# Performance work log

Measured on AMD Instinct MI355X. Metric: run time of the kernel, lower is better.

## Reference

```python
import jax, jax.numpy as jnp
from jax import lax
import numpy as np

GAMMA = 1e-4  # RBF bandwidth (init kwarg gamma)

def setup_inputs() -> dict:
    key = jax.random.key(0)
    ks = jax.random.split(key, 6)
    B, H, W = 2048, 64, 64
    P, D = 4096, 4096  # D = 4 * (H//2) * (W//2)
    NC = 10
    x = jax.random.normal(ks[0], (B, 1, H, W), dtype=jnp.float32)
    prototypes = jax.random.normal(ks[1], (P, D), dtype=jnp.float32) * 0.5
    conv_w = jax.random.normal(ks[2], (4, 1, 2, 2), dtype=jnp.float32) * 0.5
    conv_b = jax.random.normal(ks[3], (4,), dtype=jnp.float32) * 0.1
    head_w = jax.random.normal(ks[4], (NC, P), dtype=jnp.float32) * (1.0 / np.sqrt(P))
    head_b = jax.random.normal(ks[5], (NC,), dtype=jnp.float32) * 0.1
    return {"x": x, "prototypes": prototypes, "conv_w": conv_w,
            "conv_b": conv_b, "head_w": head_w, "head_b": head_b}

def reference(x, prototypes, conv_w, conv_b, head_w, head_b):
    # 2x2 stride-2 conv: [B,1,H,W] -> [B,4,H/2,W/2]
    feats = lax.conv_general_dilated(
        x, conv_w, window_strides=(2, 2), padding="VALID",
        dimension_numbers=("NCHW", "OIHW", "NCHW"))
    feats = feats + conv_b[None, :, None, None]
    B = feats.shape[0]
    feats = feats.reshape(B, -1)  # [B, D]
    # Pairwise squared distance via ||f||^2 + ||p||^2 - 2 f.p (no [B,P,D] blowup)
    f2 = jnp.sum(feats * feats, axis=1, keepdims=True)          # [B,1]
    p2 = jnp.sum(prototypes * prototypes, axis=1)[None, :]      # [1,P]
    d2 = jnp.maximum(f2 + p2 - 2.0 * feats @ prototypes.T, 0.0)  # [B,P]
    kernel_vals = jnp.exp(-GAMMA * d2)
    logits = kernel_vals @ head_w.T + head_b
    return jax.nn.log_softmax(logits, axis=-1)
```

## Files before the change

kernel.cpp:

```cpp
#include <hip/hip_runtime.h>
#include <hip/hip_bf16.h>
#include <stdint.h>

#define GAMMA 1e-4f

typedef int i32x4 __attribute__((ext_vector_type(4)));
typedef int i32x8 __attribute__((ext_vector_type(8)));
typedef float f32x4 __attribute__((ext_vector_type(4)));

__device__ __forceinline__ float bf2f(unsigned short u) {
  unsigned int x = ((unsigned int)u) << 16;
  float f; __builtin_memcpy(&f, &x, 4);
  return f;
}

__device__ __forceinline__ unsigned char f2e4m3(float x) {
  float a = fabsf(x);
  unsigned char s = x < 0.f ? 0x80 : 0;
  a = fminf(a, 448.f);
  if (a < 0.015625f) {
    int q = (int)rintf(a * 512.f);
    return s | (unsigned char)q;
  }
  unsigned int u; __builtin_memcpy(&u, &a, 4);
  u += 0x7FFFFu + ((u >> 20) & 1);
  u &= 0xFFF00000u;
  int e2 = (int)(u >> 23) - 127;
  unsigned int mant = (u >> 20) & 7;
  return s | (unsigned char)(((e2 + 7) << 3) | mant);
}

__device__ __forceinline__ unsigned int pack4(float a, float b, float c, float d) {
  return (unsigned)f2e4m3(a) | ((unsigned)f2e4m3(b) << 8) |
         ((unsigned)f2e4m3(c) << 16) | ((unsigned)f2e4m3(d) << 24);
}

__global__ __launch_bounds__(256) void prep_k(
    const float* __restrict__ x, const float* __restrict__ cw,
    const float* __restrict__ cb, unsigned char* __restrict__ fA8,
    float* __restrict__ f2, const float* __restrict__ pr,
    unsigned char* __restrict__ pB8, float* __restrict__ p2) {
  const int tid = threadIdx.x;
  __shared__ float red[4];
  if (blockIdx.x < 4096) {
    const int j = blockIdx.x;
    const float4* src = (const float4*)(pr + (size_t)j * 4096);
    float ssq = 0.f;
    unsigned int w4[4];
#pragma unroll
    for (int k = 0; k < 4; k++) {
      float4 v = src[tid * 4 + k];
      ssq += v.x * v.x + v.y * v.y + v.z * v.z + v.w * v.w;
      w4[k] = pack4(v.x, v.y, v.z, v.w);
    }
    *(uint4*)(pB8 + (size_t)j * 4096 + tid * 16) = make_uint4(w4[0], w4[1], w4[2], w4[3]);
    for (int off = 32; off > 0; off >>= 1) ssq += __shfl_down(ssq, off);
    if ((tid & 63) == 0) red[tid >> 6] = ssq;
    __syncthreads();
    if (tid == 0) p2[j] = red[0] + red[1] + red[2] + red[3];
  } else {
    const int b = blockIdx.x - 4096;
    __shared__ float swb[20];
    if (tid < 16) swb[tid] = cw[tid];
    else if (tid < 20) swb[tid] = cb[tid - 16];
    __syncthreads();
    float w[16], bias[4];
#pragma unroll
    for (int i = 0; i < 16; i++) w[i] = swb[i];
#pragma unroll
    for (int c = 0; c < 4; c++) bias[c] = swb[16 + c];
    const float* xb = x + (size_t)b * 4096;
    unsigned char* fb8 = fA8 + (size_t)b * 4096;
    const int p0 = tid * 4;
    const int h = p0 >> 5, w0 = p0 & 31;
    const float* r0 = xb + (2 * h) * 64 + 2 * w0;
    const float* r1 = r0 + 64;
    float4 a0 = *(const float4*)r0, a1 = *(const float4*)(r0 + 4);
    float4 c0 = *(const float4*)r1, c1 = *(const float4*)(r1 + 4);
    float ssq = 0.f;
#pragma unroll
    for (int c = 0; c < 4; c++) {
      float w00 = w[c * 4], w01 = w[c * 4 + 1], w10 = w[c * 4 + 2], w11 = w[c * 4 + 3];
      float v0 = bias[c] + a0.x * w00 + a0.y * w01 + c0.x * w10 + c0.y * w11;
      float v1 = bias[c] + a0.z * w00 + a0.w * w01 + c0.z * w10 + c0.w * w11;
      float v2 = bias[c] + a1.x * w00 + a1.y * w01 + c1.x * w10 + c1.y * w11;
      float v3 = bias[c] + a1.z * w00 + a1.w * w01 + c1.z * w10 + c1.w * w11;
      ssq += v0 * v0 + v1 * v1 + v2 * v2 + v3 * v3;
      *(unsigned int*)(fb8 + c * 1024 + p0) = pack4(v0, v1, v2, v3);
    }
    for (int off = 32; off > 0; off >>= 1) ssq += __shfl_down(ssq, off);
    if ((tid & 63) == 0) red[tid >> 6] = ssq;
    __syncthreads();
    if (tid == 0) f2[b] = red[0] + red[1] + red[2] + red[3];
  }
}

#define SWZA(o) ((o) ^ ((((o) >> 12) & 1) << 4))
#define SWZB(o) ((o) ^ ((((o) >> 13) & 1) << 4))
#define TILE_BYTES 49152

#define GLDS(gsrc, ldst)                                                    \
  __builtin_amdgcn_global_load_lds(                                         \
      (__attribute__((address_space(1))) void*)(void*)(gsrc),               \
      (__attribute__((address_space(3))) void*)(ldst), 16, 0, 0)

#define MFMA8(a, b, c)                                                      \
  __builtin_amdgcn_mfma_scale_f32_16x16x128_f8f6f4(                         \
      (a), (b), (c), 0, 0, 0, 0x7f7f7f7fu, 0, 0x7f7f7f7fu)

__device__ __forceinline__ i32x8 read32(const char* p0, const char* p1) {
  i32x4 lo = *(const i32x4*)p0;
  i32x4 hi = *(const i32x4*)p1;
  return __builtin_shufflevector(lo, hi, 0, 1, 2, 3, 4, 5, 6, 7);
}

#define TBODY(PTN, PTS, CA0, CA1, CA2, CA3, CB0, CB1, CB2, CB3,             \
              NA0, NA1, NA2, NA3, NB0, NB1, NB2, NB3, KB)                   \
  {                                                                         \
    asm volatile("s_waitcnt vmcnt(0)" ::: "memory");                        \
    __builtin_amdgcn_sched_barrier(0);                                      \
    __builtin_amdgcn_s_barrier();                                           \
    asm volatile("s_waitcnt lgkmcnt(0)" ::: "memory");                      \
    __builtin_amdgcn_sched_barrier(0);                                      \
    NA0 = read32((PTN) + arlo[0], (PTN) + arhi[0]);                         \
    NA1 = read32((PTN) + arlo[1], (PTN) + arhi[1]);                         \
    NA2 = read32((PTN) + arlo[2], (PTN) + arhi[2]);                         \
    NA3 = read32((PTN) + arlo[3], (PTN) + arhi[3]);                         \
    NB0 = read32((PTN) + brlo[0], (PTN) + brhi[0]);                         \
    NB1 = read32((PTN) + brlo[1], (PTN) + brhi[1]);                         \
    GLDS(agp[0] + (KB), (PTS) + aoff[0]);                                   \
    GLDS(agp[1] + (KB), (PTS) + aoff[1]);                                   \
    GLDS(bgp[0] + (KB), (PTS) + 16384 + boff[0]);                           \
    __builtin_amdgcn_sched_barrier(0);                                      \
    __builtin_amdgcn_s_setprio(1);                                          \
    acc[0][0] = MFMA8(CA0, CB0, acc[0][0]);                                 \
    acc[0][1] = MFMA8(CA0, CB1, acc[0][1]);                                 \
    acc[1][0] = MFMA8(CA1, CB0, acc[1][0]);                                 \
    acc[1][1] = MFMA8(CA1, CB1, acc[1][1]);                                 \
    acc[2][0] = MFMA8(CA2, CB0, acc[2][0]);                                 \
    acc[2][1] = MFMA8(CA2, CB1, acc[2][1]);                                 \
    acc[3][0] = MFMA8(CA3, CB0, acc[3][0]);                                 \
    acc[3][1] = MFMA8(CA3, CB1, acc[3][1]);                                 \
    __builtin_amdgcn_s_setprio(0);                                          \
    __builtin_amdgcn_sched_barrier(0);                                      \
    NB2 = read32((PTN) + brlo[2], (PTN) + brhi[2]);                         \
    NB3 = read32((PTN) + brlo[3], (PTN) + brhi[3]);                         \
    GLDS(bgp[1] + (KB), (PTS) + 16384 + boff[1]);                           \
    GLDS(bgp[2] + (KB), (PTS) + 16384 + boff[2]);                           \
    GLDS(bgp[3] + (KB), (PTS) + 16384 + boff[3]);                           \
    __builtin_amdgcn_sched_barrier(0);                                      \
    __builtin_amdgcn_s_setprio(1);                                          \
    acc[0][2] = MFMA8(CA0, CB2, acc[0][2]);                                 \
    acc[0][3] = MFMA8(CA0, CB3, acc[0][3]);                                 \
    acc[1][2] = MFMA8(CA1, CB2, acc[1][2]);                                 \
    acc[1][3] = MFMA8(CA1, CB3, acc[1][3]);                                 \
    acc[2][2] = MFMA8(CA2, CB2, acc[2][2]);                                 \
    acc[2][3] = MFMA8(CA2, CB3, acc[2][3]);                                 \
    acc[3][2] = MFMA8(CA3, CB3, acc[3][2]);                                 \
    acc[3][3] = MFMA8(CA3, CB3, acc[3][3]);                                 \
    __builtin_amdgcn_s_setprio(0);                                          \
    __builtin_amdgcn_sched_barrier(0);                                      \
  }

__global__ __launch_bounds__(512, 1) void gemm_kv_k(
    const unsigned char* __restrict__ A, const unsigned char* __restrict__ B,
    const float* __restrict__ f2, const float* __restrict__ p2,
    __hip_bfloat16* __restrict__ kv) {
  __shared__ __align__(16) char lds[3 * TILE_BYTES];
  const int tid = threadIdx.x;
  const int wave = tid >> 6, lane = tid & 63;
  const int q = lane >> 4, l16 = lane & 15;
  const int wr = wave >> 2, wc = wave & 3;

  const int wg = blockIdx.x;
  const int xcd = wg & 7, loc = wg >> 3;
  const int bm = (xcd & 1) * 8 + (loc & 7);
  const int bn = (xcd >> 1) * 4 + (loc >> 3);

  const unsigned char* agp[2];
  const unsigned char* bgp[4];
  int aoff[2], boff[4];
#pragma unroll
  for (int i = 0; i < 2; i++) {
    int phys = (tid + i * 512) * 16;
    aoff[i] = phys;
    int lg = SWZA(phys);
    int kq = lg >> 12, rw = (lg & 4095) >> 5, kl = lg & 31;
    agp[i] = A + (size_t)(bm * 128 + rw) * 4096 + kq * 32 + kl;
  }
#pragma unroll
  for (int i = 0; i < 4; i++) {
    int phys = (tid + i * 512) * 16;
    boff[i] = phys;
    int lg = SWZB(phys);
    int kq = lg >> 13, rw = (lg & 8191) >> 5, kl = lg & 31;
    bgp[i] = B + (size_t)(bn * 256 + rw) * 4096 + kq * 32 + kl;
  }

  int arlo[4], arhi[4], brlo[4], brhi[4];
#pragma unroll
  for (int m = 0; m < 4; m++) {
    int lg = q * 4096 + (wr * 64 + m * 16 + l16) * 32;
    arlo[m] = SWZA(lg);
    arhi[m] = SWZA(lg + 16);
  }
#pragma unroll
  for (int n = 0; n < 4; n++) {
    int lg = q * 8192 + (wc * 64 + n * 16 + l16) * 32;
    brlo[n] = 16384 + SWZB(lg);
    brhi[n] = 16384 + SWZB(lg + 16);
  }

  f32x4 acc[4][4] = {};
  i32x8 Xa0, Xa1, Xa2, Xa3, Xb0, Xb1, Xb2, Xb3;
  i32x8 Ya0, Ya1, Ya2, Ya3, Yb0, Yb1, Yb2, Yb3;

  char* b0 = lds;
  char* b1 = lds + TILE_BYTES;
  char* b2 = lds + 2 * TILE_BYTES;

#pragma unroll
  for (int i = 0; i < 2; i++) GLDS(agp[i], b0 + aoff[i]);
#pragma unroll
  for (int i = 0; i < 4; i++) GLDS(bgp[i], b0 + 16384 + boff[i]);
#pragma unroll
  for (int i = 0; i < 2; i++) GLDS(agp[i] + 128, b1 + aoff[i]);
#pragma unroll
  for (int i = 0; i < 4; i++) GLDS(bgp[i] + 128, b1 + 16384 + boff[i]);
  asm volatile("s_waitcnt vmcnt(6)" ::: "memory");
  __builtin_amdgcn_s_barrier();

  Xa0 = read32(b0 + arlo[0], b0 + arhi[0]);
  Xa1 = read32(b0 + arlo[1], b0 + arhi[1]);
  Xa2 = read32(b0 + arlo[2], b0 + arhi[2]);
  Xa3 = read32(b0 + arlo[3], b0 + arhi[3]);
  Xb0 = read32(b0 + brlo[0], b0 + brhi[0]);
  Xb1 = read32(b0 + brlo[1], b0 + brhi[1]);
  Xb2 = read32(b0 + brlo[2], b0 + brhi[2]);
  Xb3 = read32(b0 + brlo[3], b0 + brhi[3]);

#pragma unroll 1
  for (int t = 0; t < 32; t += 2) {
    const int kb2 = ((t + 2) & 31) * 128;
    const int kb3 = ((t + 3) & 31) * 128;
    TBODY(b1, b2, Xa0, Xa1, Xa2, Xa3, Xb0, Xb1, Xb2, Xb3,
          Ya0, Ya1, Ya2, Ya3, Yb0, Yb1, Yb2, Yb3, kb2);
    TBODY(b2, b0, Ya0, Ya1, Ya2, Ya3, Yb0, Yb1, Yb2, Yb3,
          Xa0, Xa1, Xa2, Xa3, Xb0, Xb1, Xb2, Xb3, kb3);
    char* nb0 = b2; char* nb1 = b0; char* nb2 = b1;
    b0 = nb0; b1 = nb1; b2 = nb2;
  }

  asm volatile("s_waitcnt vmcnt(0) lgkmcnt(0)" ::: "memory");

  float p2v[4];
#pragma unroll
  for (int n = 0; n < 4; n++) p2v[n] = p2[bn * 256 + wc * 64 + n * 16 + l16];
#pragma unroll
  for (int m = 0; m < 4; m++) {
#pragma unroll
    for (int j = 0; j < 4; j++) {
      int grow = bm * 128 + wr * 64 + m * 16 + q * 4 + j;
      float f2v = f2[grow];
      __hip_bfloat16* kvp = kv + (size_t)grow * 4096 + bn * 256 + wc * 64 + l16;
#pragma unroll
      for (int n = 0; n < 4; n++) {
        float d2 = fmaxf(f2v + p2v[n] - 2.0f * acc[m][n][j], 0.f);
        kvp[n * 16] = __float2bfloat16(__expf(-GAMMA * d2));
      }
    }
  }
}

__global__ __launch_bounds__(256) void head_ls_k(
    const __hip_bfloat16* __restrict__ kv, const float* __restrict__ hw,
    const float* __restrict__ hb, float* __restrict__ out) {
  const int bb = blockIdx.x * 8;
  const int tid = threadIdx.x;
  float part[8][10];
#pragma unroll
  for (int r = 0; r < 8; r++)
#pragma unroll
    for (int c = 0; c < 10; c++) part[r][c] = 0.f;
#pragma unroll
  for (int k = 0; k < 4; k++) {
    int idx = tid + k * 256;
    float4 w[10];
#pragma unroll
    for (int c = 0; c < 10; c++) w[c] = *(const float4*)(hw + c * 4096 + idx * 4);
#pragma unroll
    for (int r = 0; r < 8; r++) {
      ushort4 v = ((const ushort4*)(kv + (size_t)(bb + r) * 4096))[idx];
      float a0 = bf2f(v.x), a1 = bf2f(v.y), a2 = bf2f(v.z), a3 = bf2f(v.w);
#pragma unroll
      for (int c = 0; c < 10; c++)
        part[r][c] += a0 * w[c].x + a1 * w[c].y + a2 * w[c].z + a3 * w[c].w;
    }
  }
#pragma unroll
  for (int r = 0; r < 8; r++)
#pragma unroll
    for (int c = 0; c < 10; c++)
      for (int off = 32; off > 0; off >>= 1) part[r][c] += __shfl_down(part[r][c], off);
  __shared__ float red[4][8][10];
  if ((tid & 63) == 0) {
#pragma unroll
    for (int r = 0; r < 8; r++)
#pragma unroll
      for (int c = 0; c < 10; c++) red[tid >> 6][r][c] = part[r][c];
  }
  __syncthreads();
  if (tid < 8) {
    const int r = tid;
    float l[10], m = -1e30f;
#pragma unroll
    for (int c = 0; c < 10; c++) {
      l[c] = red[0][r][c] + red[1][r][c] + red[2][r][c] + red[3][r][c] + hb[c];
      m = fmaxf(m, l[c]);
    }
    float s = 0.f;
#pragma unroll
    for (int c = 0; c < 10; c++) s += __expf(l[c] - m);
    float lse = logf(s);
#pragma unroll
    for (int c = 0; c < 10; c++) out[(size_t)(bb + r) * 10 + c] = l[c] - m - lse;
  }
}

extern "C" void kernel_launch(void* const* d_in, const int* in_sizes, int n_in,
                              void* d_out, int out_size, void* d_ws, size_t ws_size,
                              hipStream_t stream) {
  const float* x      = (const float*)d_in[0];
  const float* protos = (const float*)d_in[1];
  const float* conv_w = (const float*)d_in[2];
  const float* conv_b = (const float*)d_in[3];
  const float* head_w = (const float*)d_in[4];
  const float* head_b = (const float*)d_in[5];
  float* out = (float*)d_out;
  char* ws = (char*)d_ws;

  unsigned char* pB8  = (unsigned char*)ws;
  unsigned char* fA8  = (unsigned char*)(ws + (16u << 20));
  __hip_bfloat16* kvb = (__hip_bfloat16*)(ws + (24u << 20));
  float* f2 = (float*)(ws + (40u << 20));
  float* p2 = (float*)(ws + (40u << 20) + 8192);

  hipLaunchKernelGGL(prep_k, dim3(6144), dim3(256), 0, stream,
                     x, conv_w, conv_b, fA8, f2, protos, pB8, p2);
  hipLaunchKernelGGL(gemm_kv_k, dim3(256), dim3(512), 0, stream, fA8, pB8, f2, p2, kvb);
  hipLaunchKernelGGL(head_ls_k, dim3(256), dim3(256), 0, stream, kvb, head_w, head_b, out);
}
```

Baseline: 95.74 us.

## Restructure FP8 GEMM main loop into four-phase interleaved LDS-read/MFMA schedule

Replaces the register double-buffered X/Y fragment scheme with a single-tile-per-iteration loop split into four phases. Each phase issues a few LDS fragment reads and global-to-LDS prefetches, then a barrier, then a small MFMA cluster. The aim is to cut register pressure and interleave LDS traffic with matrix work at finer granularity, as in published hipBLASLt-style ping-pong schedules. It adds several more workgroup barriers per K-step and exposes LDS read latency before each MFMA group, since fragments are no longer preloaded one step ahead. It also fixes the old acc[3][2] using CA3,CB3 instead of CA3,CB2.

Measured after the change: 87.57 us. 8.5% less time.

```diff
diff --git a/kernel.cpp b/kernel.cpp
--- a/kernel.cpp
+++ b/kernel.cpp
@@ -114,52 +114,75 @@
   return __builtin_shufflevector(lo, hi, 0, 1, 2, 3, 4, 5, 6, 7);
 }
 
-#define TBODY(PTN, PTS, CA0, CA1, CA2, CA3, CB0, CB1, CB2, CB3,             \
-              NA0, NA1, NA2, NA3, NB0, NB1, NB2, NB3, KB)                   \
+#define SB __builtin_amdgcn_sched_barrier(0)
+#define LGKM0 asm volatile("s_waitcnt lgkmcnt(0)" ::: "memory")
+
+#define TBODY(CUR, STG, KB)                                                 \
   {                                                                         \
-    asm volatile("s_waitcnt vmcnt(0)" ::: "memory");                        \
-    __builtin_amdgcn_sched_barrier(0);                                      \
-    __builtin_amdgcn_s_barrier();                                           \
-    asm volatile("s_waitcnt lgkmcnt(0)" ::: "memory");                      \
-    __builtin_amdgcn_sched_barrier(0);                                      \
-    NA0 = read32((PTN) + arlo[0], (PTN) + arhi[0]);                         \
-    NA1 = read32((PTN) + arlo[1], (PTN) + arhi[1]);                         \
-    NA2 = read32((PTN) + arlo[2], (PTN) + arhi[2]);                         \
-    NA3 = read32((PTN) + arlo[3], (PTN) + arhi[3]);                         \
-    NB0 = read32((PTN) + brlo[0], (PTN) + brhi[0]);                         \
-    NB1 = read32((PTN) + brlo[1], (PTN) + brhi[1]);                         \
-    GLDS(agp[0] + (KB), (PTS) + aoff[0]);                                   \
-    GLDS(agp[1] + (KB), (PTS) + aoff[1]);                                   \
-    GLDS(bgp[0] + (KB), (PTS) + 16384 + boff[0]);                           \
-    __builtin_amdgcn_sched_barrier(0);                                      \
+    i32x8 av0, av1, av2, av3, bv0, bv1, bv2, bv3;                           \
+                                                \
+    SB;                                                                     \
+    av0 = read32((CUR) + arlo[0], (CUR) + arhi[0]);                         \
+    av1 = read32((CUR) + arlo[1], (CUR) + arhi[1]);                         \
+    bv0 = read32((CUR) + brlo[0], (CUR) + brhi[0]);                         \
+    bv1 = read32((CUR) + brlo[1], (CUR) + brhi[1]);                         \
+    SB;                                                                     \
+    GLDS(agp[0] + (KB), (STG) + aoff[0]);                                   \
+    GLDS(agp[1] + (KB), (STG) + aoff[1]);                                   \
+    SB;                                                                     \
+    __builtin_amdgcn_s_barrier();                                           \
+    LGKM0; SB;                                                              \
     __builtin_amdgcn_s_setprio(1);                                          \
-    acc[0][0] = MFMA8(CA0, CB0, acc[0][0]);                                 \
-    acc[0][1] = MFMA8(CA0, CB1, acc[0][1]);                                 \
-    acc[1][0] = MFMA8(CA1, CB0, acc[1][0]);                                 \
-    acc[1][1] = MFMA8(CA1, CB1, acc[1][1]);                                 \
-    acc[2][0] = MFMA8(CA2, CB0, acc[2][0]);                                 \
-    acc[2][1] = MFMA8(CA2, CB1, acc[2][1]);                                 \
-    acc[3][0] = MFMA8(CA3, CB0, acc[3][0]);                                 \
-    acc[3][1] = MFMA8(CA3, CB1, acc[3][1]);                                 \
+    acc[0][0] = MFMA8(av0, bv0, acc[0][0]);                                 \
+    acc[0][1] = MFMA8(av0, bv1, acc[0][1]);                                 \
+    acc[1][0] = MFMA8(av1, bv0, acc[1][0]);                                 \
+    acc[1][1] = MFMA8(av1, bv1, acc[1][1]);                                 \
     __builtin_amdgcn_s_setprio(0);                                          \
-    __builtin_amdgcn_sched_barrier(0);                                      \
-    NB2 = read32((PTN) + brlo[2], (PTN) + brhi[2]);                         \
-    NB3 = read32((PTN) + brlo[3], (PTN) + brhi[3]);                         \
-    GLDS(bgp[1] + (KB), (PTS) + 16384 + boff[1]);                           \
-    GLDS(bgp[2] + (KB), (PTS) + 16384 + boff[2]);                           \
-    GLDS(bgp[3] + (KB), (PTS) + 16384 + boff[3]);                           \
-    __builtin_amdgcn_sched_barrier(0);                                      \
+    SB;                                                                     \
+                                                \
+    av2 = read32((CUR) + arlo[2], (CUR) + arhi[2]);                         \
+    av3 = read32((CUR) + arlo[3], (CUR) + arhi[3]);                         \
+    SB;                                                                     \
+    GLDS(bgp[0] + (KB), (STG) + 16384 + boff[0]);                           \
+    GLDS(bgp[1] + (KB), (STG) + 16384 + boff[1]);                           \
+    SB;                                                                     \
+    __builtin_amdgcn_s_barrier();                                           \
+    LGKM0; SB;                                                              \
     __builtin_amdgcn_s_setprio(1);                                          \
-    acc[0][2] = MFMA8(CA0, CB2, acc[0][2]);                                 \
-    acc[0][3] = MFMA8(CA0, CB3, acc[0][3]);                                 \
-    acc[1][2] = MFMA8(CA1, CB2, acc[1][2]);                                 \
-    acc[1][3] = MFMA8(CA1, CB3, acc[1][3]);                                 \
-    acc[2][2] = MFMA8(CA2, CB2, acc[2][2]);                                 \
-    acc[2][3] = MFMA8(CA2, CB3, acc[2][3]);                                 \
-    acc[3][2] = MFMA8(CA3, CB3, acc[3][2]);                                 \
-    acc[3][3] = MFMA8(CA3, CB3, acc[3][3]);                                 \
+    acc[2][0] = MFMA8(av2, bv0, acc[2][0]);                                 \
+    acc[2][1] = MFMA8(av2, bv1, acc[2][1]);                                 \
+    acc[3][0] = MFMA8(av3, bv0, acc[3][0]);                                 \
+    acc[3][1] = MFMA8(av3, bv1, acc[3][1]);                                 \
     __builtin_amdgcn_s_setprio(0);                                          \
-    __builtin_amdgcn_sched_barrier(0);                                      \
+    SB;                                                                     \
+                                                \
+    bv2 = read32((CUR) + brlo[2], (CUR) + brhi[2]);                         \
+    bv3 = read32((CUR) + brlo[3], (CUR) + brhi[3]);                         \
+    SB;                                                                     \
+    GLDS(bgp[2] + (KB), (STG) + 16384 + boff[2]);                           \
+    GLDS(bgp[3] + (KB), (STG) + 16384 + boff[3]);                           \
+    SB;                                                                     \
+    __builtin_amdgcn_s_barrier();                                           \
+    LGKM0; SB;                                                              \
+    __builtin_amdgcn_s_setprio(1);                                          \
+    acc[0][2] = MFMA8(av0, bv2, acc[0][2]);                                 \
+    acc[0][3] = MFMA8(av0, bv3, acc[0][3]);                                 \
+    acc[1][2] = MFMA8(av1, bv2, acc[1][2]);                                 \
+    acc[1][3] = MFMA8(av1, bv3, acc[1][3]);                                 \
+    __builtin_amdgcn_s_setprio(0);                                          \
+    SB;                                                                     \
+                                   \
+    __builtin_amdgcn_s_barrier();                                           \
+    __builtin_amdgcn_s_setprio(1);                                          \
+    acc[2][2] = MFMA8(av2, bv2, acc[2][2]);                                 \
+    acc[2][3] = MFMA8(av2, bv3, acc[2][3]);                                 \
+    acc[3][2] = MFMA8(av3, bv2, acc[3][2]);                                 \
+    acc[3][3] = MFMA8(av3, bv3, acc[3][3]);                                 \
+    __builtin_amdgcn_s_setprio(0);                                          \
+    SB;                                                                     \
+    asm volatile("s_waitcnt vmcnt(6)" ::: "memory");                        \
+    SB;                                                                     \
+    __builtin_amdgcn_s_barrier();                                           \
   }
 
 __global__ __launch_bounds__(512, 1) void gemm_kv_k(
@@ -212,8 +235,6 @@
   }
 
   f32x4 acc[4][4] = {};
-  i32x8 Xa0, Xa1, Xa2, Xa3, Xb0, Xb1, Xb2, Xb3;
-  i32x8 Ya0, Ya1, Ya2, Ya3, Yb0, Yb1, Yb2, Yb3;
 
   char* b0 = lds;
   char* b1 = lds + TILE_BYTES;
@@ -230,24 +251,11 @@
   asm volatile("s_waitcnt vmcnt(6)" ::: "memory");
   __builtin_amdgcn_s_barrier();
 
-  Xa0 = read32(b0 + arlo[0], b0 + arhi[0]);
-  Xa1 = read32(b0 + arlo[1], b0 + arhi[1]);
-  Xa2 = read32(b0 + arlo[2], b0 + arhi[2]);
-  Xa3 = read32(b0 + arlo[3], b0 + arhi[3]);
-  Xb0 = read32(b0 + brlo[0], b0 + brhi[0]);
-  Xb1 = read32(b0 + brlo[1], b0 + brhi[1]);
-  Xb2 = read32(b0 + brlo[2], b0 + brhi[2]);
-  Xb3 = read32(b0 + brlo[3], b0 + brhi[3]);
-
 #pragma unroll 1
-  for (int t = 0; t < 32; t += 2) {
+  for (int t = 0; t < 32; ++t) {
     const int kb2 = ((t + 2) & 31) * 128;
-    const int kb3 = ((t + 3) & 31) * 128;
-    TBODY(b1, b2, Xa0, Xa1, Xa2, Xa3, Xb0, Xb1, Xb2, Xb3,
-          Ya0, Ya1, Ya2, Ya3, Yb0, Yb1, Yb2, Yb3, kb2);
-    TBODY(b2, b0, Ya0, Ya1, Ya2, Ya3, Yb0, Yb1, Yb2, Yb3,
-          Xa0, Xa1, Xa2, Xa3, Xb0, Xb1, Xb2, Xb3, kb3);
-    char* nb0 = b2; char* nb1 = b0; char* nb2 = b1;
+    TBODY(b0, b2, kb2);
+    char* nb0 = b1; char* nb1 = b2; char* nb2 = b0;
     b0 = nb0; b1 = nb1; b2 = nb2;
   }
 
```
